# Optimization experiments

Hardware: AMD Instinct MI355X
Metric: run time of the kernel (lower is better)

The kernel has to match this reference:

```python
import jax, jax.numpy as jnp
import numpy as np

N = 8192          # nodes
E = 262144        # edges (avg degree 32)
IN = 32           # output_seq_len * in_channels
HID = 16          # hidden_channels
HEADS = 8
OUT = 32          # output_seq_len * out_channels
SLOPE = 0.2       # GATv2 leaky_relu negative_slope
EPS = 1e-12       # F.normalize eps


def setup_inputs() -> dict:
    key = jax.random.key(0)
    ks = jax.random.split(key, 12)
    g = lambda k, shape, fan: (jax.random.normal(k, shape, jnp.float32) / np.float32(np.sqrt(fan)))
    x = jax.random.normal(ks[0], (N, IN), jnp.float32)
    edge_index = jax.random.randint(ks[1], (2, E), 0, N, dtype=jnp.int64)
    # conv1: in=IN -> HEADS x HID, concat
    W1l = g(ks[2], (IN, HEADS * HID), IN)
    b1l = jnp.zeros((HEADS * HID,), jnp.float32)
    W1r = g(ks[3], (IN, HEADS * HID), IN)
    b1r = jnp.zeros((HEADS * HID,), jnp.float32)
    att1 = g(ks[4], (HEADS, HID), HID)
    bias1 = jnp.zeros((HEADS * HID,), jnp.float32)
    W2l = g(ks[5], (HEADS * HID, OUT), HEADS * HID)
    b2l = jnp.zeros((OUT,), jnp.float32)
    W2r = g(ks[6], (HEADS * HID, OUT), HEADS * HID)
    b2r = jnp.zeros((OUT,), jnp.float32)
    att2 = g(ks[7], (1, OUT), OUT)
    bias2 = jnp.zeros((OUT,), jnp.float32)
    return {"x": x, "edge_index": edge_index,
            "W1l": W1l, "b1l": b1l, "W1r": W1r, "b1r": b1r, "att1": att1, "bias1": bias1,
            "W2l": W2l, "b2l": b2l, "W2r": W2r, "b2r": b2r, "att2": att2, "bias2": bias2}


def gatv2_conv(x, src, dst, Wl, bl, Wr, br, att, bias, heads, C, concat):
    """GATv2Conv (eval mode, self-loops already in src/dst). x: [N, F]."""
    n = x.shape[0]
    xl = (x @ Wl + bl).reshape(n, heads, C)  # source transform
    xr = (x @ Wr + br).reshape(n, heads, C)  # target transform
    h = jax.nn.leaky_relu(xl[src] + xr[dst], SLOPE)        # [Etot, H, C]
    e = jnp.einsum('ehc,hc->eh', h, att)                    # [Etot, H]
    m = jax.ops.segment_max(e, dst, num_segments=n)         # stable softmax per target
    p = jnp.exp(e - m[dst])
    s = jax.ops.segment_sum(p, dst, num_segments=n)
    alpha = p / (s[dst] + 1e-16)                            # [Etot, H]
    out = jax.ops.segment_sum(alpha[:, :, None] * xl[src], dst, num_segments=n)  # [n, H, C]
    out = out.reshape(n, heads * C) if concat else out.mean(axis=1)
    return out + bias


def reference(x, edge_index, W1l, b1l, W1r, b1r, att1, bias1, W2l, b2l, W2r, b2r, att2, bias2):
    n = x.shape[0]
    loops = jnp.arange(n, dtype=edge_index.dtype)
    src = jnp.concatenate([edge_index[0], loops])
    dst = jnp.concatenate([edge_index[1], loops])
    h1 = gatv2_conv(x, src, dst, W1l, b1l, W1r, b1r, att1, bias1, HEADS, HID, True)
    h2 = gatv2_conv(h1, src, dst, W2l, b2l, W2r, b2r, att2, bias2, 1, OUT, False)
    norm = jnp.sqrt(jnp.sum(h2 * h2, axis=1, keepdims=True))
    z = h2 / jnp.maximum(norm, EPS)                         # F.normalize(p=2, dim=1)
    A_pred = jax.nn.sigmoid(z @ z.T)                        # [N, N]
    return (A_pred, z)
```

## Files before the change

### kernel.cpp

```cpp
#include <hip/hip_runtime.h>
#include <hip/hip_bf16.h>
#include <cstdint>
#include <cstddef>

typedef float f32x4 __attribute__((ext_vector_type(4)));
typedef short short8 __attribute__((ext_vector_type(8)));

#define SLOT_SHIFT 7

__device__ __forceinline__ float bf2f(ushort u){ return __uint_as_float(((unsigned)u) << 16); }
__device__ __forceinline__ float lrelu(float v){ return fmaxf(v, 0.2f*v); }

__global__ __launch_bounds__(256) void k_lin1_scatter(const float* __restrict__ x,
                          const float* __restrict__ W1l, const float* __restrict__ b1l,
                          const float* __restrict__ W1r, const float* __restrict__ b1r,
                          __hip_bfloat16* __restrict__ xl1b, float* __restrict__ xr1,
                          const int* __restrict__ ei, int E, int N,
                          int* __restrict__ cnt, int* __restrict__ ssrc, int NL){
  int bid = blockIdx.x, t = threadIdx.x;
  if (bid < NL){
    __shared__ float xs[32][32];
    int sub = t >> 7, f = t & 127;
    int r0 = bid*32;
    float wl[32], wr[32];
    #pragma unroll
    for (int k = 0; k < 32; k++){ wl[k] = W1l[k*128 + f]; wr[k] = W1r[k*128 + f]; }
    float bl = b1l[f], br = b1r[f];
    #pragma unroll
    for (int i = 0; i < 4; i++){
      int idx = t + i*256;
      xs[idx >> 5][idx & 31] = x[r0*32 + idx];
    }
    __syncthreads();
    #pragma unroll 4
    for (int rr = 0; rr < 16; rr++){
      int r = sub*16 + rr;
      float al = bl, ar = br;
      const float4* xv4 = (const float4*)xs[r];
      #pragma unroll
      for (int q = 0; q < 8; q++){
        float4 xv = xv4[q];
        al += xv.x*wl[q*4+0] + xv.y*wl[q*4+1] + xv.z*wl[q*4+2] + xv.w*wl[q*4+3];
        ar += xv.x*wr[q*4+0] + xv.y*wr[q*4+1] + xv.z*wr[q*4+2] + xv.w*wr[q*4+3];
      }
      xl1b[(size_t)(r0+r)*128 + f] = __float2bfloat16(al);
      xr1[(size_t)(r0+r)*128 + f] = ar;
    }
  } else {
    int i = (bid - NL)*256 + t;
    int tot = E + N;
    if (i < tot){
      int s = (i < E) ? ei[i]     : (i - E);
      int d = (i < E) ? ei[E + i] : (i - E);
      int pos = atomicAdd(&cnt[d], 1);
      ssrc[(d << SLOT_SHIFT) + pos] = s;
    }
  }
}

__global__ __launch_bounds__(256) void k_conv1l2(const int* __restrict__ cnt,
                       const int* __restrict__ ssrc,
                       const __hip_bfloat16* __restrict__ xl1b, const float* __restrict__ xr1,
                       const float* __restrict__ att1, const float* __restrict__ bias1,
                       const float* __restrict__ W2l, const float* __restrict__ b2l,
                       const float* __restrict__ W2r, const float* __restrict__ b2r,
                       __hip_bfloat16* __restrict__ xl2b, float* __restrict__ xr2){
  __shared__ float p_s[2][128][8];
  __shared__ int   sj[2][128];
  __shared__ float h1s[4][128];
  int t = threadIdx.x;
  int sub = t >> 7, f = t & 127;
  int hp = f & 7;
  const ushort* xb = (const ushort*)xl1b;
  float4 attr0 = *(const float4*)(att1 + hp*16);
  float4 attr1 = *(const float4*)(att1 + hp*16 + 4);
  float4 attr2 = *(const float4*)(att1 + hp*16 + 8);
  float4 attr3 = *(const float4*)(att1 + hp*16 + 12);
  float b1f = bias1[f];
  int d0 = blockIdx.x*4;
  #pragma unroll
  for (int it = 0; it < 2; it++){
    int d = d0 + it*2 + sub;
    int j0 = d << SLOT_SHIFT;
    int deg = cnt[d];
    float4 xr0v = *(const float4*)(xr1 + (size_t)d*128 + hp*16);
    float4 xr1v = *(const float4*)(xr1 + (size_t)d*128 + hp*16 + 4);
    float4 xr2v = *(const float4*)(xr1 + (size_t)d*128 + hp*16 + 8);
    float4 xr3v = *(const float4*)(xr1 + (size_t)d*128 + hp*16 + 12);
    __syncthreads();
    for (int i = f; i < deg; i += 128) sj[sub][i] = ssrc[j0 + i];
    __syncthreads();
    int npair = deg*8;
    for (int pr = f; pr < npair; pr += 128){
      int jj = pr >> 3;
      int src = sj[sub][jj];
      const short8* vp = (const short8*)(xb + (size_t)src*128 + hp*16);
      short8 v0 = vp[0], v1 = vp[1];
      float e, tv = 0.f;
      e = bf2f((ushort)v0[0]) + xr0v.x; tv += lrelu(e)*attr0.x;
      e = bf2f((ushort)v0[1]) + xr0v.y; tv += lrelu(e)*attr0.y;
      e = bf2f((ushort)v0[2]) + xr0v.z; tv += lrelu(e)*attr0.z;
      e = bf2f((ushort)v0[3]) + xr0v.w; tv += lrelu(e)*attr0.w;
      e = bf2f((ushort)v0[4]) + xr1v.x; tv += lrelu(e)*attr1.x;
      e = bf2f((ushort)v0[5]) + xr1v.y; tv += lrelu(e)*attr1.y;
      e = bf2f((ushort)v0[6]) + xr1v.z; tv += lrelu(e)*attr1.z;
      e = bf2f((ushort)v0[7]) + xr1v.w; tv += lrelu(e)*attr1.w;
      e = bf2f((ushort)v1[0]) + xr2v.x; tv += lrelu(e)*attr2.x;
      e = bf2f((ushort)v1[1]) + xr2v.y; tv += lrelu(e)*attr2.y;
      e = bf2f((ushort)v1[2]) + xr2v.z; tv += lrelu(e)*attr2.z;
      e = bf2f((ushort)v1[3]) + xr2v.w; tv += lrelu(e)*attr2.w;
      e = bf2f((ushort)v1[4]) + xr3v.x; tv += lrelu(e)*attr3.x;
      e = bf2f((ushort)v1[5]) + xr3v.y; tv += lrelu(e)*attr3.y;
      e = bf2f((ushort)v1[6]) + xr3v.z; tv += lrelu(e)*attr3.z;
      e = bf2f((ushort)v1[7]) + xr3v.w; tv += lrelu(e)*attr3.w;
      p_s[sub][jj][hp] = __expf(tv);
    }
    __syncthreads();
    int h2 = f >> 4;
    float s = 0.f, acc = 0.f;
    int jj = 0;
    for (; jj + 3 < deg; jj += 4){
      int4 s4 = *(const int4*)&sj[sub][jj];
      float p0 = p_s[sub][jj+0][h2];
      float p1 = p_s[sub][jj+1][h2];
      float p2 = p_s[sub][jj+2][h2];
      float p3 = p_s[sub][jj+3][h2];
      float x0 = bf2f(xb[(size_t)s4.x*128 + f]);
      float x1 = bf2f(xb[(size_t)s4.y*128 + f]);
      float x2 = bf2f(xb[(size_t)s4.z*128 + f]);
      float x3 = bf2f(xb[(size_t)s4.w*128 + f]);
      s   += (p0 + p1) + (p2 + p3);
      acc += p0*x0 + p1*x1 + p2*x2 + p3*x3;
    }
    for (; jj < deg; jj++){
      int src = sj[sub][jj];
      float p = p_s[sub][jj][h2];
      float x = bf2f(xb[(size_t)src*128 + f]);
      s += p; acc += p*x;
    }
    h1s[it*2 + sub][f] = acc/(s + 1e-16f) + b1f;
  }
  __syncthreads();
  {
    int r = t >> 6;
    int idx = t & 63;
    int c = idx & 31; bool left = idx < 32;
    const float* W = left ? W2l : W2r;
    float a = left ? b2l[c] : b2r[c];
    #pragma unroll 8
    for (int kk = 0; kk < 128; kk++) a += h1s[r][kk] * W[kk*32 + c];
    int d = d0 + r;
    if (left) xl2b[(size_t)d*32 + c] = __float2bfloat16(a);
    else      xr2[(size_t)d*32 + c] = a;
  }
}

__global__ __launch_bounds__(256) void k_conv2(const int* __restrict__ cnt,
                       const int* __restrict__ ssrc,
                       const __hip_bfloat16* __restrict__ xl2b, const float* __restrict__ xr2,
                       const float* __restrict__ att2, const float* __restrict__ bias2,
                       float* __restrict__ z, __hip_bfloat16* __restrict__ zb){
  __shared__ float p_s[4][128];
  __shared__ int   sj[4][128];
  __shared__ float xr_s[4][32];
  __shared__ float att_s[32];
  int t = threadIdx.x;
  int w = t >> 6, lane = t & 63;
  int d = blockIdx.x*4 + w;
  int j0 = d << SLOT_SHIFT;
  int deg = cnt[d];
  if (t < 32) att_s[t] = att2[t];
  if (lane < 32) xr_s[w][lane] = xr2[(size_t)d*32 + lane];
  __syncthreads();
  const ushort* xb = (const ushort*)xl2b;
  for (int jj = lane; jj < deg; jj += 64){
    int src = ssrc[j0 + jj];
    sj[w][jj] = src;
    const short8* vp = (const short8*)(xb + (size_t)src*32);
    short8 v0 = vp[0], v1 = vp[1], v2 = vp[2], v3 = vp[3];
    float tv = 0.f;
    #pragma unroll
    for (int k = 0; k < 8; k++){
      float e0 = bf2f((ushort)v0[k]) + xr_s[w][k];      tv += lrelu(e0)*att_s[k];
      float e1 = bf2f((ushort)v1[k]) + xr_s[w][8+k];    tv += lrelu(e1)*att_s[8+k];
      float e2 = bf2f((ushort)v2[k]) + xr_s[w][16+k];   tv += lrelu(e2)*att_s[16+k];
      float e3 = bf2f((ushort)v3[k]) + xr_s[w][24+k];   tv += lrelu(e3)*att_s[24+k];
    }
    p_s[w][jj] = __expf(tv);
  }
  __syncthreads();
  int half = lane >> 5, c = lane & 31;
  float s0 = 0.f, a0 = 0.f, s1 = 0.f, a1 = 0.f;
  int jj = half;
  for (; jj + 2 < deg; jj += 4){
    int srcA = sj[w][jj], srcB = sj[w][jj+2];
    float pA = p_s[w][jj], pB = p_s[w][jj+2];
    float xA = bf2f(xb[(size_t)srcA*32 + c]);
    float xB = bf2f(xb[(size_t)srcB*32 + c]);
    s0 += pA; a0 += pA*xA;
    s1 += pB; a1 += pB*xB;
  }
  for (; jj < deg; jj += 2){
    int src = sj[w][jj];
    float p = p_s[w][jj];
    float x = bf2f(xb[(size_t)src*32 + c]);
    s0 += p; a0 += p*x;
  }
  float s = s0 + s1, acc = a0 + a1;
  s   += __shfl_xor(s, 32, 64);
  acc += __shfl_xor(acc, 32, 64);
  float v = acc/(s + 1e-16f) + bias2[c];
  float ss = v*v;
  #pragma unroll
  for (int k = 1; k < 32; k <<= 1) ss += __shfl_xor(ss, k, 64);
  if (half == 0){
    float zv = v / fmaxf(sqrtf(ss), 1e-12f);
    z[(size_t)d*32 + c] = zv;
    zb[(size_t)d*32 + c] = __float2bfloat16(zv);
  }
}

__global__ __launch_bounds__(256) void k_adj(const __hip_bfloat16* __restrict__ zb,
                                             float* __restrict__ out, int N){
  __shared__ float tile[64][68];
  int tid = threadIdx.x;
  int w = tid >> 6, l = tid & 63;
  int hi = l >> 4, lo = l & 15;
  int r0 = blockIdx.y*64, c0 = blockIdx.x*64;
  short8 a = *(const short8*)(zb + (size_t)(r0 + w*16 + lo)*32 + hi*8);
  f32x4 acc[4];
  #pragma unroll
  for (int ct = 0; ct < 4; ct++){
    short8 b = *(const short8*)(zb + (size_t)(c0 + ct*16 + lo)*32 + hi*8);
    acc[ct] = __builtin_amdgcn_mfma_f32_16x16x32_bf16(a, b, (f32x4){0.f,0.f,0.f,0.f}, 0, 0, 0);
  }
  #pragma unroll
  for (int ct = 0; ct < 4; ct++){
    #pragma unroll
    for (int r = 0; r < 4; r++)
      tile[w*16 + hi*4 + r][ct*16 + lo] = 1.f/(1.f + __expf(-acc[ct][r]));
  }
  __syncthreads();
  #pragma unroll
  for (int k = 0; k < 4; k++){
    int g = tid + k*256;
    int row = g >> 4, c4 = (g & 15)*4;
    f32x4 v = *(const f32x4*)&tile[row][c4];
    *(f32x4*)&out[(size_t)(r0 + row)*N + c0 + c4] = v;
  }
}

extern "C" void kernel_launch(void* const* d_in, const int* in_sizes, int n_in,
                              void* d_out, int out_size, void* d_ws, size_t ws_size,
                              hipStream_t stream){
  const float* x     = (const float*)d_in[0];
  const int*   ei    = (const int*)  d_in[1];
  const float* W1l   = (const float*)d_in[2];
  const float* b1l   = (const float*)d_in[3];
  const float* W1r   = (const float*)d_in[4];
  const float* b1r   = (const float*)d_in[5];
  const float* att1  = (const float*)d_in[6];
  const float* bias1 = (const float*)d_in[7];
  const float* W2l   = (const float*)d_in[8];
  const float* b2l   = (const float*)d_in[9];
  const float* W2r   = (const float*)d_in[10];
  const float* b2r   = (const float*)d_in[11];
  const float* att2  = (const float*)d_in[12];
  const float* bias2 = (const float*)d_in[13];

  const int N = in_sizes[0] / 32;
  const int E = in_sizes[1] / 2;
  const int Etot = E + N;

  char* w = (char*)d_ws;
  size_t p = 0;
  auto take = [&](size_t bytes)->char*{
    char* r = w + p;
    p = (p + bytes + 255) & ~(size_t)255;
    return r;
  };
  int*   cnt  = (int*)  take((size_t)N*4);
  int*   ssrc = (int*)  take(((size_t)N << SLOT_SHIFT)*4);
  __hip_bfloat16* xl1b = (__hip_bfloat16*)take((size_t)N*128*2);
  float* xr1  = (float*)take((size_t)N*128*4);
  __hip_bfloat16* xl2b = (__hip_bfloat16*)take((size_t)N*32*2);
  float* xr2  = (float*)take((size_t)N*32*4);
  __hip_bfloat16* zb = (__hip_bfloat16*)take((size_t)N*32*2);

  float* Apred = (float*)d_out;
  float* z     = Apred + (size_t)N*N;

  const int NL = N/32;
  const int NS = (Etot + 255)/256;
  (void)hipMemsetAsync(cnt, 0, (size_t)N*4, stream);
  k_lin1_scatter<<<NL + NS, 256, 0, stream>>>(x, W1l, b1l, W1r, b1r, xl1b, xr1,
                                              ei, E, N, cnt, ssrc, NL);
  k_conv1l2<<<N/4, 256, 0, stream>>>(cnt, ssrc, xl1b, xr1, att1, bias1,
                                     W2l, b2l, W2r, b2r, xl2b, xr2);
  k_conv2  <<<N/4, 256, 0, stream>>>(cnt, ssrc, xl2b, xr2, att2, bias2, z, zb);

  dim3 grid(N/64, N/64);
  k_adj    <<<grid, 256, 0, stream>>>(zb, Apred, N);
}
```

Measured before the change: 113.7 us.

## Fuse GATv2 layer-1 attention scoring with aggregation in registers, reduce partials via LDS

The conv1 kernel now has each thread handle one (edge-group, head) pair, computing the attention logit and immediately accumulating p*x over 16 channels in registers from the same bf16 source row it already loaded. This removes the second gather pass over xl1 and the per-edge probability buffer in shared memory. Partial sums from 16 edge groups are then reduced through a padded LDS array. The sigmoid in the adjacency kernel also switches to a hardware reciprocal. The trade-off is higher register pressure and a softmax computed without max subtraction, as before.

Result: faster. 105.5 us, median of 2 (-7.2%).

```diff
diff --git a/kernel.cpp b/kernel.cpp
--- a/kernel.cpp
+++ b/kernel.cpp
@@ -65,78 +65,61 @@
                        const float* __restrict__ W2l, const float* __restrict__ b2l,
                        const float* __restrict__ W2r, const float* __restrict__ b2r,
                        __hip_bfloat16* __restrict__ xl2b, float* __restrict__ xr2){
-  __shared__ float p_s[2][128][8];
+  __shared__ float pLDS[2][16][8][17];
   __shared__ int   sj[2][128];
   __shared__ float h1s[4][128];
   int t = threadIdx.x;
   int sub = t >> 7, f = t & 127;
-  int hp = f & 7;
+  int jgrp = f >> 3, hp = f & 7;
   const ushort* xb = (const ushort*)xl1b;
-  float4 attr0 = *(const float4*)(att1 + hp*16);
-  float4 attr1 = *(const float4*)(att1 + hp*16 + 4);
-  float4 attr2 = *(const float4*)(att1 + hp*16 + 8);
-  float4 attr3 = *(const float4*)(att1 + hp*16 + 12);
+  float attv[16];
+  #pragma unroll
+  for (int q = 0; q < 16; q++) attv[q] = att1[hp*16 + q];
   float b1f = bias1[f];
+  int h2 = f >> 4, q2 = f & 15;
   int d0 = blockIdx.x*4;
   #pragma unroll
   for (int it = 0; it < 2; it++){
     int d = d0 + it*2 + sub;
     int j0 = d << SLOT_SHIFT;
     int deg = cnt[d];
-    float4 xr0v = *(const float4*)(xr1 + (size_t)d*128 + hp*16);
-    float4 xr1v = *(const float4*)(xr1 + (size_t)d*128 + hp*16 + 4);
-    float4 xr2v = *(const float4*)(xr1 + (size_t)d*128 + hp*16 + 8);
-    float4 xr3v = *(const float4*)(xr1 + (size_t)d*128 + hp*16 + 12);
+    float xrv[16];
+    #pragma unroll
+    for (int q = 0; q < 16; q++) xrv[q] = xr1[(size_t)d*128 + hp*16 + q];
     __syncthreads();
     for (int i = f; i < deg; i += 128) sj[sub][i] = ssrc[j0 + i];
     __syncthreads();
-    int npair = deg*8;
-    for (int pr = f; pr < npair; pr += 128){
-      int jj = pr >> 3;
+    float facc[16];
+    #pragma unroll
+    for (int q = 0; q < 16; q++) facc[q] = 0.f;
+    float sacc = 0.f;
+    for (int jj = jgrp; jj < deg; jj += 16){
       int src = sj[sub][jj];
       const short8* vp = (const short8*)(xb + (size_t)src*128 + hp*16);
       short8 v0 = vp[0], v1 = vp[1];
-      float e, tv = 0.f;
-      e = bf2f((ushort)v0[0]) + xr0v.x; tv += lrelu(e)*attr0.x;
-      e = bf2f((ushort)v0[1]) + xr0v.y; tv += lrelu(e)*attr0.y;
-      e = bf2f((ushort)v0[2]) + xr0v.z; tv += lrelu(e)*attr0.z;
-      e = bf2f((ushort)v0[3]) + xr0v.w; tv += lrelu(e)*attr0.w;
-      e = bf2f((ushort)v0[4]) + xr1v.x; tv += lrelu(e)*attr1.x;
-      e = bf2f((ushort)v0[5]) + xr1v.y; tv += lrelu(e)*attr1.y;
-      e = bf2f((ushort)v0[6]) + xr1v.z; tv += lrelu(e)*attr1.z;
-      e = bf2f((ushort)v0[7]) + xr1v.w; tv += lrelu(e)*attr1.w;
-      e = bf2f((ushort)v1[0]) + xr2v.x; tv += lrelu(e)*attr2.x;
-      e = bf2f((ushort)v1[1]) + xr2v.y; tv += lrelu(e)*attr2.y;
-      e = bf2f((ushort)v1[2]) + xr2v.z; tv += lrelu(e)*attr2.z;
-      e = bf2f((ushort)v1[3]) + xr2v.w; tv += lrelu(e)*attr2.w;
-      e = bf2f((ushort)v1[4]) + xr3v.x; tv += lrelu(e)*attr3.x;
-      e = bf2f((ushort)v1[5]) + xr3v.y; tv += lrelu(e)*attr3.y;
-      e = bf2f((ushort)v1[6]) + xr3v.z; tv += lrelu(e)*attr3.z;
-      e = bf2f((ushort)v1[7]) + xr3v.w; tv += lrelu(e)*attr3.w;
-      p_s[sub][jj][hp] = __expf(tv);
-    }
-    __syncthreads();
-    int h2 = f >> 4;
+      float xv[16];
+      #pragma unroll
+      for (int k = 0; k < 8; k++){
+        xv[k]   = bf2f((ushort)v0[k]);
+        xv[8+k] = bf2f((ushort)v1[k]);
+      }
+      float tv = 0.f;
+      #pragma unroll
+      for (int q = 0; q < 16; q++) tv += lrelu(xv[q] + xrv[q]) * attv[q];
+      float p = __expf(tv);
+      sacc += p;
+      #pragma unroll
+      for (int q = 0; q < 16; q++) facc[q] += p * xv[q];
+    }
+    #pragma unroll
+    for (int q = 0; q < 16; q++) pLDS[sub][jgrp][hp][q] = facc[q];
+    pLDS[sub][jgrp][hp][16] = sacc;
+    __syncthreads();
     float s = 0.f, acc = 0.f;
-    int jj = 0;
-    for (; jj + 3 < deg; jj += 4){
-      int4 s4 = *(const int4*)&sj[sub][jj];
-      float p0 = p_s[sub][jj+0][h2];
-      float p1 = p_s[sub][jj+1][h2];
-      float p2 = p_s[sub][jj+2][h2];
-      float p3 = p_s[sub][jj+3][h2];
-      float x0 = bf2f(xb[(size_t)s4.x*128 + f]);
-      float x1 = bf2f(xb[(size_t)s4.y*128 + f]);
-      float x2 = bf2f(xb[(size_t)s4.z*128 + f]);
-      float x3 = bf2f(xb[(size_t)s4.w*128 + f]);
-      s   += (p0 + p1) + (p2 + p3);
-      acc += p0*x0 + p1*x1 + p2*x2 + p3*x3;
-    }
-    for (; jj < deg; jj++){
-      int src = sj[sub][jj];
-      float p = p_s[sub][jj][h2];
-      float x = bf2f(xb[(size_t)src*128 + f]);
-      s += p; acc += p*x;
+    #pragma unroll
+    for (int g = 0; g < 16; g++){
+      acc += pLDS[sub][g][h2][q2];
+      s   += pLDS[sub][g][h2][16];
     }
     h1s[it*2 + sub][f] = acc/(s + 1e-16f) + b1f;
   }
@@ -238,7 +221,7 @@
   for (int ct = 0; ct < 4; ct++){
     #pragma unroll
     for (int r = 0; r < 4; r++)
-      tile[w*16 + hi*4 + r][ct*16 + lo] = 1.f/(1.f + __expf(-acc[ct][r]));
+      tile[w*16 + hi*4 + r][ct*16 + lo] = __builtin_amdgcn_rcpf(1.f + __expf(-acc[ct][r]));
   }
   __syncthreads();
   #pragma unroll
```
